# Kernel optimization log

Hardware: AMD Instinct MI355X
Metric: run time of the kernel (lower is better)

## Reference

```python
import jax, jax.numpy as jnp
import numpy as np

E = 512
H = 8
D = E // H
HID = 2048
NE = 4
TOPK = 2
EPS = 1e-5
NEG = -1e9


def _ln(x, w, b):
    mu = jnp.mean(x, axis=-1, keepdims=True)
    var = jnp.mean(jnp.square(x - mu), axis=-1, keepdims=True)
    return (x - mu) * jax.lax.rsqrt(var + EPS) * w + b


def _expert(xf, mask, ln1_w, ln1_b, ipw, ipb, opw, opb, ln2_w, ln2_b, w1, b1, w2, b2):
    # xf: [T, E]; mask: [T] bool (allowed keys = routed tokens)
    T = xf.shape[0]
    h = _ln(xf, ln1_w, ln1_b)
    qkv = h @ ipw.T + ipb                       # [T, 3E]
    q, k, v = jnp.split(qkv, 3, axis=-1)
    q = q.reshape(T, H, D).transpose(1, 0, 2)   # [H, T, D]
    k = k.reshape(T, H, D).transpose(1, 0, 2)
    v = v.reshape(T, H, D).transpose(1, 0, 2)
    scores = jnp.einsum('htd,hsd->hts', q, k) / jnp.sqrt(jnp.asarray(D, xf.dtype))
    scores = jnp.where(mask[None, None, :], scores, NEG)
    a = jax.nn.softmax(scores, axis=-1)
    o = jnp.einsum('hts,hsd->htd', a, v).transpose(1, 0, 2).reshape(T, E)
    o = o @ opw.T + opb
    x1 = xf + o                                 # residual (dropout = identity, eval)
    h2 = _ln(x1, ln2_w, ln2_b)
    m = jax.nn.gelu(h2 @ w1.T + b1, approximate=False) @ w2.T + b2
    return x1 + m


def setup_inputs() -> dict:
    key = jax.random.key(0)
    ks = jax.random.split(key, 16)
    s = 0.02
    inp = {
        'x': jax.random.normal(ks[0], (4, 512, E), dtype=jnp.float32),
        'gate_w': jax.random.normal(ks[1], (NE, E), dtype=jnp.float32) * s,
        'gate_b': jnp.zeros((NE,), jnp.float32),
        'ln1_w': jnp.ones((NE, E), jnp.float32),
        'ln1_b': jnp.zeros((NE, E), jnp.float32),
        'in_proj_w': jax.random.normal(ks[2], (NE, 3 * E, E), dtype=jnp.float32) * s,
        'in_proj_b': jnp.zeros((NE, 3 * E), jnp.float32),
        'out_proj_w': jax.random.normal(ks[3], (NE, E, E), dtype=jnp.float32) * s,
        'out_proj_b': jnp.zeros((NE, E), jnp.float32),
        'ln2_w': jnp.ones((NE, E), jnp.float32),
        'ln2_b': jnp.zeros((NE, E), jnp.float32),
        'mlp_w1': jax.random.normal(ks[4], (NE, HID, E), dtype=jnp.float32) * s,
        'mlp_b1': jnp.zeros((NE, HID), jnp.float32),
        'mlp_w2': jax.random.normal(ks[5], (NE, E, HID), dtype=jnp.float32) * s,
        'mlp_b2': jnp.zeros((NE, E), jnp.float32),
    }
    return inp


def reference(x, gate_w, gate_b, ln1_w, ln1_b, in_proj_w, in_proj_b, out_proj_w,
              out_proj_b, ln2_w, ln2_b, mlp_w1, mlp_b1, mlp_w2, mlp_b2):
    B, N, _ = x.shape
    T = B * N
    xf = x.reshape(T, E)
    logits = xf @ gate_w.T + gate_b                      # [T, NE]
    topk_val, topk_idx = jax.lax.top_k(logits, TOPK)
    probs = jax.nn.softmax(topk_val, axis=-1)            # [T, TOPK]
    out = jnp.zeros_like(xf)
    for kk in range(TOPK):
        idx = topk_idx[:, kk]
        w = probs[:, kk][:, None]
        for e in range(NE):
            mask = idx == e
            eo = _expert(xf, mask,
                         ln1_w[e], ln1_b[e], in_proj_w[e], in_proj_b[e],
                         out_proj_w[e], out_proj_b[e], ln2_w[e], ln2_b[e],
                         mlp_w1[e], mlp_b1[e], mlp_w2[e], mlp_b2[e])
            out = out + jnp.where(mask[:, None], eo * w, 0.0)
    return out.reshape(B, N, E)
```

## Files before the change

kernel.cpp:

```cpp
#include <hip/hip_runtime.h>
#include <hip/hip_bf16.h>

#define T_TOK 2048
#define E_DIM 512
#define NHEAD 8
#define DHEAD 64
#define HID_D 2048
#define NEXP 4
#define NROW_ (2 * T_TOK)
#define VT_STRIDE 4352

typedef short short8 __attribute__((ext_vector_type(8)));
typedef float floatx4 __attribute__((ext_vector_type(4)));

__device__ __forceinline__ void gld16(const void* g, void* l) {
  __builtin_amdgcn_global_load_lds((const __attribute__((address_space(1))) void*)g,
                                   (__attribute__((address_space(3))) void*)l, 16, 0, 0);
}

__device__ inline float wave_sum(float v) {
  for (int off = 32; off > 0; off >>= 1) v += __shfl_xor(v, off);
  return v;
}

__device__ __forceinline__ unsigned pack_bf2(float a, float b) {
  __hip_bfloat16 ha = __float2bfloat16(a), hb = __float2bfloat16(b);
  unsigned ua = *(unsigned short*)&ha, ub = *(unsigned short*)&hb;
  return ua | (ub << 16);
}

__device__ __forceinline__ void cvt4(const float* __restrict__ s, __hip_bfloat16* __restrict__ d,
                                     int i4, int n) {
  if (i4 < n) {
    float4 v = *reinterpret_cast<const float4*>(s + i4);
    __hip_bfloat16 tmp[4] = {__float2bfloat16(v.x), __float2bfloat16(v.y),
                             __float2bfloat16(v.z), __float2bfloat16(v.w)};
    *reinterpret_cast<ushort4*>(d + i4) = *reinterpret_cast<const ushort4*>(tmp);
  }
}

__global__ void cvt_weights(const float* __restrict__ s0, const float* __restrict__ s1,
                            const float* __restrict__ s2, const float* __restrict__ s3,
                            __hip_bfloat16* d0, __hip_bfloat16* d1,
                            __hip_bfloat16* d2, __hip_bfloat16* d3,
                            int n0, int n1, int n2, int n3) {
  int i4 = (blockIdx.x * 256 + threadIdx.x) * 4;
  cvt4(s0, d0, i4, n0);
  cvt4(s1, d1, i4, n1);
  cvt4(s2, d2, i4, n2);
  cvt4(s3, d3, i4, n3);
}

__global__ void gate_kernel(const float* __restrict__ x, const float* __restrict__ gw,
                            const float* __restrict__ gb, int* token_e, float* token_p) {
  int wid = threadIdx.x >> 6, lane = threadIdx.x & 63;
  int t = blockIdx.x * 4 + wid;
  float a0 = 0, a1 = 0, a2 = 0, a3 = 0;
  for (int i = 0; i < 8; i++) {
    int c = lane + 64 * i;
    float xv = x[(size_t)t * E_DIM + c];
    a0 += xv * gw[0 * E_DIM + c];
    a1 += xv * gw[1 * E_DIM + c];
    a2 += xv * gw[2 * E_DIM + c];
    a3 += xv * gw[3 * E_DIM + c];
  }
  a0 = wave_sum(a0); a1 = wave_sum(a1); a2 = wave_sum(a2); a3 = wave_sum(a3);
  if (lane == 0) {
    float lg[4] = {a0 + gb[0], a1 + gb[1], a2 + gb[2], a3 + gb[3]};
    int i0 = 0;
    for (int e = 1; e < 4; e++) if (lg[e] > lg[i0]) i0 = e;
    int i1 = -1;
    for (int e = 0; e < 4; e++) {
      if (e == i0) continue;
      if (i1 < 0 || lg[e] > lg[i1]) i1 = e;
    }
    float e1 = __expf(lg[i1] - lg[i0]);
    float inv = 1.f / (1.f + e1);
    token_e[t] = i0; token_e[T_TOK + t] = i1;
    token_p[t] = inv; token_p[T_TOK + t] = e1 * inv;
  }
}

__global__ void count_kernel(const int* __restrict__ token_e, int* counts) {
  int g = blockIdx.x, kk = g >> 2, e = g & 3;
  __shared__ int ws4[4];
  int tid = threadIdx.x, wid = tid >> 6, lane = tid & 63;
  int c = 0;
  for (int t = tid; t < T_TOK; t += 256) c += (token_e[kk * T_TOK + t] == e);
  for (int off = 32; off; off >>= 1) c += __shfl_xor(c, off);
  if (lane == 0) ws4[wid] = c;
  __syncthreads();
  if (tid == 0) counts[g] = ws4[0] + ws4[1] + ws4[2] + ws4[3];
}

__global__ void offs_kernel(const int* __restrict__ counts, int* offs, int* padoffs) {
  int o = 0, po = 0;
  offs[0] = 0; padoffs[0] = 0;
  for (int g = 0; g < 8; g++) {
    o += counts[g]; offs[g + 1] = o;
    po += (counts[g] + 31) & ~31; padoffs[g + 1] = po;
  }
}

__global__ void compact_kernel(const int* __restrict__ token_e, const int* __restrict__ offs,
                               const int* __restrict__ padoffs, int* perm, int* rowg,
                               int* pmap, int* invrow) {
  int g = blockIdx.x, kk = g >> 2, e = g & 3;
  __shared__ int wcnt[4];
  __shared__ int base;
  int tid = threadIdx.x, wid = tid >> 6, lane = tid & 63;
  int og = offs[g], pg = padoffs[g];
  if (tid == 0) base = 0;
  __syncthreads();
  for (int t0 = 0; t0 < T_TOK; t0 += 256) {
    int t = t0 + tid;
    bool pred = token_e[kk * T_TOK + t] == e;
    unsigned long long mask = __ballot(pred);
    int rank = __popcll(mask & ((1ull << lane) - 1ull));
    if (lane == 0) wcnt[wid] = __popcll(mask);
    __syncthreads();
    int woff = 0;
    for (int i = 0; i < wid; i++) woff += wcnt[i];
    if (pred) {
      int row = og + base + woff + rank;
      perm[row] = t;
      rowg[row] = g;
      pmap[row] = pg + (row - og);
      invrow[kk * T_TOK + t] = row;
    }
    __syncthreads();
    if (tid == 0) base += wcnt[0] + wcnt[1] + wcnt[2] + wcnt[3];
    __syncthreads();
  }
}

__global__ void ln_kernel(const float* __restrict__ src, const int* __restrict__ perm,
                          const int* __restrict__ rowg, const float* __restrict__ lnw,
                          const float* __restrict__ lnb, __hip_bfloat16* __restrict__ dst) {
  int wid = threadIdx.x >> 6, lane = threadIdx.x & 63;
  int row = blockIdx.x * 4 + wid;
  int e = rowg[row] & 3;
  const float* xr = src + (size_t)(perm ? perm[row] : row) * E_DIM;
  float v[8];
  float s = 0;
  for (int i = 0; i < 8; i++) { v[i] = xr[lane + 64 * i]; s += v[i]; }
  s = wave_sum(s);
  float mu = s * (1.f / 512.f);
  float q = 0;
  for (int i = 0; i < 8; i++) { float d = v[i] - mu; q += d * d; }
  q = wave_sum(q);
  float rstd = rsqrtf(q * (1.f / 512.f) + 1e-5f);
  for (int i = 0; i < 8; i++) {
    int c = lane + 64 * i;
    dst[(size_t)row * E_DIM + c] =
        __float2bfloat16((v[i] - mu) * rstd * lnw[e * E_DIM + c] + lnb[e * E_DIM + c]);
  }
}

__global__ void transpose_v(const short* __restrict__ v, const int* __restrict__ pmap,
                            short* __restrict__ vT) {
  __shared__ short tile[64][65];
  int r0 = blockIdx.x * 64, c0 = blockIdx.y * 64;
  int tc = threadIdx.x & 63, tr4 = threadIdx.x >> 6;
  for (int i = 0; i < 64; i += 4)
    tile[tr4 + i][tc] = v[(size_t)(r0 + tr4 + i) * E_DIM + c0 + tc];
  __syncthreads();
  int pcol = pmap[r0 + tc];
  for (int i = 0; i < 64; i += 4)
    vT[(size_t)(c0 + tr4 + i) * VT_STRIDE + pcol] = tile[tc][tr4 + i];
}

__global__ void zero_gaps(const int* __restrict__ offs, const int* __restrict__ padoffs,
                          short* __restrict__ vT) {
  int g = blockIdx.x;
  int cnt = offs[g + 1] - offs[g];
  int gap = (padoffs[g + 1] - padoffs[g]) - cnt;
  if ((int)threadIdx.x < gap) {
    int col = padoffs[g] + cnt + threadIdx.x;
    for (int d = blockIdx.y; d < E_DIM; d += gridDim.y)
      vT[(size_t)d * VT_STRIDE + col] = 0;
  }
}

__global__ __launch_bounds__(256) void attn_mfma(
    const short* __restrict__ qb, const short* __restrict__ kb,
    const short* __restrict__ vT, const int* __restrict__ offs,
    const int* __restrict__ padoffs, __hip_bfloat16* __restrict__ ob) {
  int d0 = blockIdx.x;
  int g = d0 & 7;
  int rem = d0 >> 3;
  int h = rem >> 5;
  int qblk = rem & 31;
  int sbeg = offs[g], rend = offs[g + 1];
  int q0 = sbeg + qblk * 64;
  if (q0 >= rend) return;
  int G = rend - sbeg;
  int pg = padoffs[g];
  int tid = threadIdx.x, wid = tid >> 6, lane = tid & 63;
  int fr = lane & 15, lg = lane >> 4;
  int qw = q0 + wid * 16;

  __shared__ short Kt[2][32 * 64];
  __shared__ short Vt[2][64 * 32];

  int arow = qw + fr; if (arow > rend - 1) arow = rend - 1;
  const short* qp = qb + (size_t)arow * E_DIM + h * DHEAD;
  short8 qf0 = *reinterpret_cast<const short8*>(qp + lg * 8);
  short8 qf1 = *reinterpret_cast<const short8*>(qp + 32 + lg * 8);

  int offB = tid * 16;
  int krow = offB >> 7, kinner = offB & 127;
  int ksrc = (kinner ^ ((krow & 7) << 4)) >> 1;
  int vL = offB ^ (((offB >> 7) & 7) << 4);
  int vd = vL >> 6, vkey0 = (vL & 63) >> 1;
  int wb = wid * 512;
  const short* vrow = vT + (size_t)(h * DHEAD + vd) * VT_STRIDE + pg;

  auto stage = [&](int buf, int kbase) {
    int gr = sbeg + kbase + krow; if (gr > NROW_ - 1) gr = NROW_ - 1;
    gld16(kb + (size_t)gr * E_DIM + h * DHEAD + ksrc, &Kt[buf][wb]);
    gld16(vrow + kbase + vkey0, &Vt[buf][wb]);
  };

  floatx4 acc[4] = {};
  float m_r = -1e30f, l_r = 0.f;

  stage(0, 0);
  asm volatile("s_waitcnt vmcnt(0)" ::: "memory");
  __syncthreads();

  int cur = 0;
  for (int kbase = 0; kbase < G; kbase += 32) {
    if (kbase + 32 < G) stage(cur ^ 1, kbase + 32);
    const char* Kb = (const char*)&Kt[cur][0];
    const char* Vb = (const char*)&Vt[cur][0];

    int r0r = fr, r1r = 16 + fr;
    short8 kf00 = *reinterpret_cast<const short8*>(Kb + r0r * 128 + ((lg * 16) ^ ((r0r & 7) << 4)));
    short8 kf01 = *reinterpret_cast<const short8*>(Kb + r0r * 128 + ((64 + lg * 16) ^ ((r0r & 7) << 4)));
    short8 kf10 = *reinterpret_cast<const short8*>(Kb + r1r * 128 + ((lg * 16) ^ ((r1r & 7) << 4)));
    short8 kf11 = *reinterpret_cast<const short8*>(Kb + r1r * 128 + ((64 + lg * 16) ^ ((r1r & 7) << 4)));

    floatx4 s0 = {}, s1 = {};
    s0 = __builtin_amdgcn_mfma_f32_16x16x32_bf16(kf00, qf0, s0, 0, 0, 0);
    s0 = __builtin_amdgcn_mfma_f32_16x16x32_bf16(kf01, qf1, s0, 0, 0, 0);
    s1 = __builtin_amdgcn_mfma_f32_16x16x32_bf16(kf10, qf0, s1, 0, 0, 0);
    s1 = __builtin_amdgcn_mfma_f32_16x16x32_bf16(kf11, qf1, s1, 0, 0, 0);

    float sv[8];
    float mloc = -1e30f;
#pragma unroll
    for (int j = 0; j < 4; j++) {
      int k0 = kbase + lg * 4 + j;
      sv[j] = (k0 < G) ? s0[j] * 0.125f : -1e30f;
      sv[4 + j] = (k0 + 16 < G) ? s1[j] * 0.125f : -1e30f;
      mloc = fmaxf(mloc, fmaxf(sv[j], sv[4 + j]));
    }
    mloc = fmaxf(mloc, __shfl_xor(mloc, 16));
    mloc = fmaxf(mloc, __shfl_xor(mloc, 32));
    if (__any(mloc > m_r + 8.f)) {
      float mn = fmaxf(m_r, mloc);
      float corr = __expf(m_r - mn);
      m_r = mn;
      l_r *= corr;
      float cq0 = __shfl(corr, lg * 4 + 0), cq1 = __shfl(corr, lg * 4 + 1);
      float cq2 = __shfl(corr, lg * 4 + 2), cq3 = __shfl(corr, lg * 4 + 3);
#pragma unroll
      for (int db = 0; db < 4; db++) {
        acc[db][0] *= cq0; acc[db][1] *= cq1; acc[db][2] *= cq2; acc[db][3] *= cq3;
      }
    }
    float p[8], sl = 0.f;
#pragma unroll
    for (int i = 0; i < 8; i++) { p[i] = __expf(sv[i] - m_r); sl += p[i]; }
    sl += __shfl_xor(sl, 16);
    sl += __shfl_xor(sl, 32);
    l_r += sl;

    union { unsigned u[4]; short8 s8; } pa0, pa1;
    pa0.u[0] = pack_bf2(p[0], p[1]); pa0.u[1] = pack_bf2(p[2], p[3]);
    pa0.u[2] = 0; pa0.u[3] = 0;
    pa1.u[0] = pack_bf2(p[4], p[5]); pa1.u[1] = pack_bf2(p[6], p[7]);
    pa1.u[2] = 0; pa1.u[3] = 0;

#pragma unroll
    for (int db = 0; db < 4; db++) {
      int dd = db * 16 + fr;
      int s = ((dd >> 1) & 7) << 4;
      uint2 w0 = *reinterpret_cast<const uint2*>(Vb + ((dd * 64 + lg * 8) ^ s));
      uint2 w1 = *reinterpret_cast<const uint2*>(Vb + ((dd * 64 + 32 + lg * 8) ^ s));
      union { unsigned u[4]; short8 s8; } bv0, bv1;
      bv0.u[0] = w0.x; bv0.u[1] = w0.y; bv0.u[2] = 0; bv0.u[3] = 0;
      bv1.u[0] = w1.x; bv1.u[1] = w1.y; bv1.u[2] = 0; bv1.u[3] = 0;
      acc[db] = __builtin_amdgcn_mfma_f32_16x16x32_bf16(pa0.s8, bv0.s8, acc[db], 0, 0, 0);
      acc[db] = __builtin_amdgcn_mfma_f32_16x16x32_bf16(pa1.s8, bv1.s8, acc[db], 0, 0, 0);
    }

    asm volatile("s_waitcnt vmcnt(0)" ::: "memory");
    __syncthreads();
    cur ^= 1;
  }

  float lq0 = __shfl(l_r, lg * 4 + 0), lq1 = __shfl(l_r, lg * 4 + 1);
  float lq2 = __shfl(l_r, lg * 4 + 2), lq3 = __shfl(l_r, lg * 4 + 3);
  float lq[4] = {lq0, lq1, lq2, lq3};
#pragma unroll
  for (int db = 0; db < 4; db++)
#pragma unroll
    for (int j = 0; j < 4; j++) {
      int row = qw + lg * 4 + j;
      if (row < rend)
        ob[(size_t)row * E_DIM + h * DHEAD + db * 16 + fr] = __float2bfloat16(acc[db][j] / lq[j]);
    }
}

template <int MODE>
__global__ __launch_bounds__(256) void gemm_mfma(
    const short* __restrict__ A, const short* __restrict__ Wb,
    const float* __restrict__ bias, const int* __restrict__ offs,
    const int* __restrict__ perm, const float* __restrict__ resid,
    __hip_bfloat16* __restrict__ bq, __hip_bfloat16* __restrict__ bk,
    __hip_bfloat16* __restrict__ bv, float* __restrict__ outf,
    float* __restrict__ outf2) {
  constexpr int K = (MODE == 3) ? HID_D : E_DIM;
  constexpr int N = (MODE == 0) ? 3 * E_DIM : (MODE == 2) ? HID_D : E_DIM;
  constexpr bool SPLIT = (MODE == 3);
  constexpr int KLEN = SPLIT ? K / 2 : K;
  constexpr int NKSTEP = KLEN / 64;
  constexpr int NXB = 32;
  __shared__ short Abuf[3][4096];
  __shared__ short Bbuf[3][4096];

  int d = blockIdx.x;
  int g = d & 7;
  int rem = d >> 3;
  int ksel = 0;
  if constexpr (SPLIT) { ksel = rem & 1; rem >>= 1; }
  int yb = rem / NXB, xb = rem % NXB;
  int e = g & 3;
  int rbeg = offs[g], rend = offs[g + 1];
  int row0 = rbeg + xb * 64;
  if (row0 >= rend) return;
  int col0 = yb * 64;
  int kbeg = ksel * KLEN;
  int tid = threadIdx.x;
  int wid = tid >> 6, lane = tid & 63;
  int wm = wid >> 1, wn = wid & 1;
  int fr = lane & 15, lg = lane >> 4;
  const short* wbase = Wb + (size_t)e * N * K;

  int st_row[2], st_src[2], st_arow[2];
  int wavebase = wid << 9;
  for (int c = 0; c < 2; c++) {
    int off = c * 4096 + tid * 16;
    int trow = off >> 7;
    int inner = off & 127;
    st_row[c] = trow;
    st_src[c] = (inner ^ ((trow & 7) << 4)) >> 1;
    int ga = row0 + trow;
    st_arow[c] = ga < rend ? ga : rend - 1;
  }

  auto stage = [&](int buf, int kb) {
#pragma unroll
    for (int c = 0; c < 2; c++) {
      gld16(A + (size_t)st_arow[c] * K + kb + st_src[c], &Abuf[buf][c * 2048 + wavebase]);
      gld16(wbase + (size_t)(col0 + st_row[c]) * K + kb + st_src[c],
            &Bbuf[buf][c * 2048 + wavebase]);
    }
  };

  floatx4 acc[2][2] = {};
  stage(0, kbeg);
  stage(1, kbeg + 64);
  asm volatile("s_waitcnt vmcnt(4)" ::: "memory");
  __builtin_amdgcn_s_barrier();
  __builtin_amdgcn_sched_barrier(0);

  int bcur = 0;
  for (int t = 0; t < NKSTEP; ++t) {
    int b2 = bcur + 2; if (b2 >= 3) b2 -= 3;
    if (t + 2 < NKSTEP) stage(b2, kbeg + (t + 2) * 64);
    const char* Ab = (const char*)&Abuf[bcur][0];
    const char* Bb = (const char*)&Bbuf[bcur][0];
    short8 af[2][2], bf8[2][2];
#pragma unroll
    for (int mi = 0; mi < 2; mi++)
#pragma unroll
      for (int ks = 0; ks < 2; ks++) {
        int row = wm * 32 + mi * 16 + fr;
        int cb = ks * 64 + lg * 16;
        af[mi][ks] = *reinterpret_cast<const short8*>(Ab + row * 128 + (cb ^ ((row & 7) << 4)));
      }
#pragma unroll
    for (int ni = 0; ni < 2; ni++)
#pragma unroll
      for (int ks = 0; ks < 2; ks++) {
        int row = wn * 32 + ni * 16 + fr;
        int cb = ks * 64 + lg * 16;
        bf8[ni][ks] = *reinterpret_cast<const short8*>(Bb + row * 128 + (cb ^ ((row & 7) << 4)));
      }
#pragma unroll
    for (int mi = 0; mi < 2; mi++)
#pragma unroll
      for (int ni = 0; ni < 2; ni++) {
        acc[mi][ni] = __builtin_amdgcn_mfma_f32_16x16x32_bf16(af[mi][0], bf8[ni][0], acc[mi][ni], 0, 0, 0);
        acc[mi][ni] = __builtin_amdgcn_mfma_f32_16x16x32_bf16(af[mi][1], bf8[ni][1], acc[mi][ni], 0, 0, 0);
      }
    if (t + 1 < NKSTEP) {
      if (t + 2 < NKSTEP) asm volatile("s_waitcnt vmcnt(4)" ::: "memory");
      else                asm volatile("s_waitcnt vmcnt(0)" ::: "memory");
      asm volatile("s_waitcnt lgkmcnt(0)" ::: "memory");
      __builtin_amdgcn_s_barrier();
      __builtin_amdgcn_sched_barrier(0);
    }
    bcur = (bcur + 1 == 3) ? 0 : bcur + 1;
  }

  for (int mi = 0; mi < 2; mi++)
    for (int ni = 0; ni < 2; ni++)
      for (int j = 0; j < 4; j++) {
        int row = row0 + wm * 32 + mi * 16 + lg * 4 + j;
        if (row >= rend) continue;
        int col = col0 + wn * 32 + ni * 16 + fr;
        float val = acc[mi][ni][j];
        if constexpr (MODE != 3) val += bias[e * N + col];
        if constexpr (MODE == 0) {
          if (col < E_DIM) bq[(size_t)row * E_DIM + col] = __float2bfloat16(val);
          else if (col < 2 * E_DIM) bk[(size_t)row * E_DIM + col - E_DIM] = __float2bfloat16(val);
          else bv[(size_t)row * E_DIM + col - 2 * E_DIM] = __float2bfloat16(val);
        } else if constexpr (MODE == 1) {
          int t = perm[row];
          outf[(size_t)row * E_DIM + col] = val + resid[(size_t)t * E_DIM + col];
        } else if constexpr (MODE == 2) {
          float gl = 0.5f * val * (1.f + erff(val * 0.70710678118654752f));
          bq[(size_t)row * HID_D + col] = __float2bfloat16(gl);
        } else {
          if (ksel == 0) {
            val += bias[e * N + col] + resid[(size_t)row * E_DIM + col];
            outf[(size_t)row * E_DIM + col] = val;
          } else {
            outf2[(size_t)row * E_DIM + col] = val;
          }
        }
      }
}

__global__ void combine_kernel(const float* __restrict__ y1, const float* __restrict__ y2,
                               const int* __restrict__ invrow,
                               const float* __restrict__ token_p, float* __restrict__ out) {
  int t = blockIdx.x;
  int r0 = invrow[t], r1 = invrow[T_TOK + t];
  float p0 = token_p[t], p1 = token_p[T_TOK + t];
  const float* a0 = y1 + (size_t)r0 * E_DIM;
  const float* b0 = y2 + (size_t)r0 * E_DIM;
  const float* a1 = y1 + (size_t)r1 * E_DIM;
  const float* b1 = y2 + (size_t)r1 * E_DIM;
  float* o = out + (size_t)t * E_DIM;
  for (int i = threadIdx.x; i < E_DIM; i += 256)
    o[i] = p0 * (a0[i] + b0[i]) + p1 * (a1[i] + b1[i]);
}

extern "C" void kernel_launch(void* const* d_in, const int* in_sizes, int n_in,
                              void* d_out, int out_size, void* d_ws, size_t ws_size,
                              hipStream_t stream) {
  const float* x      = (const float*)d_in[0];
  const float* gate_w = (const float*)d_in[1];
  const float* gate_b = (const float*)d_in[2];
  const float* ln1_w  = (const float*)d_in[3];
  const float* ln1_b  = (const float*)d_in[4];
  const float* ipw    = (const float*)d_in[5];
  const float* ipb    = (const float*)d_in[6];
  const float* opw    = (const float*)d_in[7];
  const float* opb    = (const float*)d_in[8];
  const float* ln2_w  = (const float*)d_in[9];
  const float* ln2_b  = (const float*)d_in[10];
  const float* w1     = (const float*)d_in[11];
  const float* b1     = (const float*)d_in[12];
  const float* w2     = (const float*)d_in[13];
  const float* b2     = (const float*)d_in[14];
  float* out = (float*)d_out;

  const int SZ_IP = NEXP * 3 * E_DIM * E_DIM;
  const int SZ_OP = NEXP * E_DIM * E_DIM;
  const int SZ_W1 = NEXP * HID_D * E_DIM;
  const int SZ_W2 = NEXP * E_DIM * HID_D;
  const int NROW = NROW_;

  char* ws = (char*)d_ws;
  size_t off = 0;
  auto carve = [&](size_t bytes) -> void* {
    void* p = ws + off;
    off += (bytes + 255) & ~(size_t)255;
    return p;
  };
  __hip_bfloat16* ipw_bf = (__hip_bfloat16*)carve((size_t)SZ_IP * 2);
  __hip_bfloat16* opw_bf = (__hip_bfloat16*)carve((size_t)SZ_OP * 2);
  __hip_bfloat16* w1_bf  = (__hip_bfloat16*)carve((size_t)SZ_W1 * 2);
  __hip_bfloat16* w2_bf  = (__hip_bfloat16*)carve((size_t)SZ_W2 * 2);
  __hip_bfloat16* h_bf   = (__hip_bfloat16*)carve((size_t)NROW * E_DIM * 2);
  __hip_bfloat16* q_bf   = (__hip_bfloat16*)carve((size_t)NROW * E_DIM * 2);
  __hip_bfloat16* k_bf   = (__hip_bfloat16*)carve((size_t)NROW * E_DIM * 2);
  __hip_bfloat16* v_bf   = (__hip_bfloat16*)carve((size_t)NROW * E_DIM * 2);
  __hip_bfloat16* o_bf   = (__hip_bfloat16*)carve((size_t)NROW * E_DIM * 2);
  __hip_bfloat16* h2_bf  = (__hip_bfloat16*)carve((size_t)NROW * E_DIM * 2);
  __hip_bfloat16* mid_bf = (__hip_bfloat16*)carve((size_t)NROW * HID_D * 2);
  short* vT     = (short*)carve((size_t)E_DIM * VT_STRIDE * 2);
  float* x1     = (float*)carve((size_t)NROW * E_DIM * 4);
  int* token_e  = (int*)carve((size_t)NROW * 4);
  float* token_p= (float*)carve((size_t)NROW * 4);
  int* perm     = (int*)carve((size_t)NROW * 4);
  int* rowg     = (int*)carve((size_t)NROW * 4);
  int* pmap     = (int*)carve((size_t)NROW * 4);
  int* invrow   = (int*)carve((size_t)NROW * 4);
  int* counts   = (int*)carve(8 * 4);
  int* offs     = (int*)carve(9 * 4);
  int* padoffs  = (int*)carve(9 * 4);
  float* ybuf  = (float*)h_bf;
  float* ybuf2 = (float*)k_bf;

  cvt_weights<<<SZ_W1 / 4 / 256, 256, 0, stream>>>(ipw, opw, w1, w2, ipw_bf, opw_bf,
                                                   w1_bf, w2_bf, SZ_IP, SZ_OP, SZ_W1, SZ_W2);
  gate_kernel<<<T_TOK / 4, 256, 0, stream>>>(x, gate_w, gate_b, token_e, token_p);
  count_kernel<<<8, 256, 0, stream>>>(token_e, counts);
  offs_kernel<<<1, 1, 0, stream>>>(counts, offs, padoffs);
  compact_kernel<<<8, 256, 0, stream>>>(token_e, offs, padoffs, perm, rowg, pmap, invrow);
  ln_kernel<<<NROW / 4, 256, 0, stream>>>(x, perm, rowg, ln1_w, ln1_b, h_bf);
  gemm_mfma<0><<<8 * 24 * 32, 256, 0, stream>>>((const short*)h_bf, (const short*)ipw_bf,
      ipb, offs, perm, nullptr, q_bf, k_bf, v_bf, nullptr, nullptr);
  transpose_v<<<dim3(NROW / 64, E_DIM / 64), 256, 0, stream>>>((const short*)v_bf, pmap, vT);
  zero_gaps<<<dim3(8, 64), 32, 0, stream>>>(offs, padoffs, vT);
  attn_mfma<<<8 * 8 * 32, 256, 0, stream>>>((const short*)q_bf, (const short*)k_bf,
      vT, offs, padoffs, o_bf);
  gemm_mfma<1><<<8 * 8 * 32, 256, 0, stream>>>((const short*)o_bf, (const short*)opw_bf,
      opb, offs, perm, x, nullptr, nullptr, nullptr, x1, nullptr);
  ln_kernel<<<NROW / 4, 256, 0, stream>>>(x1, nullptr, rowg, ln2_w, ln2_b, h2_bf);
  gemm_mfma<2><<<8 * 32 * 32, 256, 0, stream>>>((const short*)h2_bf, (const short*)w1_bf,
      b1, offs, perm, nullptr, mid_bf, nullptr, nullptr, nullptr, nullptr);
  gemm_mfma<3><<<8 * 2 * 8 * 32, 256, 0, stream>>>((const short*)mid_bf, (const short*)w2_bf,
      b2, offs, perm, x1, nullptr, nullptr, nullptr, ybuf, ybuf2);
  combine_kernel<<<T_TOK, 256, 0, stream>>>(ybuf, ybuf2, invrow, token_p, out);
  (void)in_sizes; (void)n_in; (void)ws_size;
}
```

Baseline: 183.6 us.

## Triple-buffer 64-key attention tiles, fuse routing kernels, vectorise combine

The attention kernel now processes 64 keys per iteration with a three-stage LDS ring, prefetching two tiles ahead with partial vmcnt waits and raising wave priority around the MFMA sections. This cuts barrier and loop overhead per key and hides more load latency. The count, offset and compact kernels are merged into one route kernel that each block recomputes redundantly, removing two launches. The combine kernel switches to float4 with 128 threads, and the vT padding moves to 64-row alignment, which needs zero_gaps widened to 64 threads. The larger LDS footprint may lower occupancy.

```diff
diff --git a/kernel.cpp b/kernel.cpp
--- a/kernel.cpp
+++ b/kernel.cpp
@@ -8,7 +8,7 @@
 #define HID_D 2048
 #define NEXP 4
 #define NROW_ (2 * T_TOK)
-#define VT_STRIDE 4352
+#define VT_STRIDE 4608
 
 typedef short short8 __attribute__((ext_vector_type(8)));
 typedef float floatx4 __attribute__((ext_vector_type(4)));
@@ -81,35 +81,30 @@
   }
 }
 
-__global__ void count_kernel(const int* __restrict__ token_e, int* counts) {
+__global__ void route_kernel(const int* __restrict__ token_e, int* perm, int* rowg,
+                             int* pmap, int* invrow, int* offs_out, int* padoffs_out) {
   int g = blockIdx.x, kk = g >> 2, e = g & 3;
-  __shared__ int ws4[4];
   int tid = threadIdx.x, wid = tid >> 6, lane = tid & 63;
-  int c = 0;
-  for (int t = tid; t < T_TOK; t += 256) c += (token_e[kk * T_TOK + t] == e);
-  for (int off = 32; off; off >>= 1) c += __shfl_xor(c, off);
-  if (lane == 0) ws4[wid] = c;
+  __shared__ int cnt_s[8][4];
+  for (int gg = 0; gg < 8; gg++) {
+    int kk2 = gg >> 2, e2 = gg & 3;
+    int c = 0;
+    for (int t = tid; t < T_TOK; t += 256) c += (token_e[kk2 * T_TOK + t] == e2);
+    for (int off = 32; off; off >>= 1) c += __shfl_xor(c, off);
+    if (lane == 0) cnt_s[gg][wid] = c;
+  }
   __syncthreads();
-  if (tid == 0) counts[g] = ws4[0] + ws4[1] + ws4[2] + ws4[3];
-}
-
-__global__ void offs_kernel(const int* __restrict__ counts, int* offs, int* padoffs) {
-  int o = 0, po = 0;
+  int offs[9], padoffs[9];
   offs[0] = 0; padoffs[0] = 0;
-  for (int g = 0; g < 8; g++) {
-    o += counts[g]; offs[g + 1] = o;
-    po += (counts[g] + 31) & ~31; padoffs[g + 1] = po;
-  }
-}
-
-__global__ void compact_kernel(const int* __restrict__ token_e, const int* __restrict__ offs,
-                               const int* __restrict__ padoffs, int* perm, int* rowg,
-                               int* pmap, int* invrow) {
-  int g = blockIdx.x, kk = g >> 2, e = g & 3;
+  for (int gg = 0; gg < 8; gg++) {
+    int c = cnt_s[gg][0] + cnt_s[gg][1] + cnt_s[gg][2] + cnt_s[gg][3];
+    offs[gg + 1] = offs[gg] + c;
+    padoffs[gg + 1] = padoffs[gg] + ((c + 63) & ~63);
+  }
+  if (g == 0 && tid < 9) { offs_out[tid] = offs[tid]; padoffs_out[tid] = padoffs[tid]; }
+  int og = offs[g], pg = padoffs[g];
   __shared__ int wcnt[4];
   __shared__ int base;
-  int tid = threadIdx.x, wid = tid >> 6, lane = tid & 63;
-  int og = offs[g], pg = padoffs[g];
   if (tid == 0) base = 0;
   __syncthreads();
   for (int t0 = 0; t0 < T_TOK; t0 += 256) {
@@ -200,62 +195,78 @@
   int fr = lane & 15, lg = lane >> 4;
   int qw = q0 + wid * 16;
 
-  __shared__ short Kt[2][32 * 64];
-  __shared__ short Vt[2][64 * 32];
+  __shared__ short Kt[3][64 * 64];
+  __shared__ short Vt[3][64 * 64];
 
   int arow = qw + fr; if (arow > rend - 1) arow = rend - 1;
   const short* qp = qb + (size_t)arow * E_DIM + h * DHEAD;
   short8 qf0 = *reinterpret_cast<const short8*>(qp + lg * 8);
   short8 qf1 = *reinterpret_cast<const short8*>(qp + 32 + lg * 8);
 
-  int offB = tid * 16;
-  int krow = offB >> 7, kinner = offB & 127;
-  int ksrc = (kinner ^ ((krow & 7) << 4)) >> 1;
-  int vL = offB ^ (((offB >> 7) & 7) << 4);
-  int vd = vL >> 6, vkey0 = (vL & 63) >> 1;
-  int wb = wid * 512;
-  const short* vrow = vT + (size_t)(h * DHEAD + vd) * VT_STRIDE + pg;
+  int st_row[2], st_src[2];
+  int wb = wid << 9;
+  for (int c = 0; c < 2; c++) {
+    int off = c * 4096 + tid * 16;
+    int row = off >> 7, inner = off & 127;
+    st_row[c] = row;
+    st_src[c] = (inner ^ ((row & 7) << 4)) >> 1;
+  }
 
   auto stage = [&](int buf, int kbase) {
-    int gr = sbeg + kbase + krow; if (gr > NROW_ - 1) gr = NROW_ - 1;
-    gld16(kb + (size_t)gr * E_DIM + h * DHEAD + ksrc, &Kt[buf][wb]);
-    gld16(vrow + kbase + vkey0, &Vt[buf][wb]);
+#pragma unroll
+    for (int c = 0; c < 2; c++) {
+      int gr = sbeg + kbase + st_row[c]; if (gr > NROW_ - 1) gr = NROW_ - 1;
+      gld16(kb + (size_t)gr * E_DIM + h * DHEAD + st_src[c], &Kt[buf][c * 2048 + wb]);
+      gld16(vT + (size_t)(h * DHEAD + st_row[c]) * VT_STRIDE + pg + kbase + st_src[c],
+            &Vt[buf][c * 2048 + wb]);
+    }
   };
 
   floatx4 acc[4] = {};
   float m_r = -1e30f, l_r = 0.f;
+  int nt = (G + 63) >> 6;
 
   stage(0, 0);
-  asm volatile("s_waitcnt vmcnt(0)" ::: "memory");
-  __syncthreads();
-
-  int cur = 0;
-  for (int kbase = 0; kbase < G; kbase += 32) {
-    if (kbase + 32 < G) stage(cur ^ 1, kbase + 32);
-    const char* Kb = (const char*)&Kt[cur][0];
-    const char* Vb = (const char*)&Vt[cur][0];
-
-    int r0r = fr, r1r = 16 + fr;
-    short8 kf00 = *reinterpret_cast<const short8*>(Kb + r0r * 128 + ((lg * 16) ^ ((r0r & 7) << 4)));
-    short8 kf01 = *reinterpret_cast<const short8*>(Kb + r0r * 128 + ((64 + lg * 16) ^ ((r0r & 7) << 4)));
-    short8 kf10 = *reinterpret_cast<const short8*>(Kb + r1r * 128 + ((lg * 16) ^ ((r1r & 7) << 4)));
-    short8 kf11 = *reinterpret_cast<const short8*>(Kb + r1r * 128 + ((64 + lg * 16) ^ ((r1r & 7) << 4)));
-
-    floatx4 s0 = {}, s1 = {};
-    s0 = __builtin_amdgcn_mfma_f32_16x16x32_bf16(kf00, qf0, s0, 0, 0, 0);
-    s0 = __builtin_amdgcn_mfma_f32_16x16x32_bf16(kf01, qf1, s0, 0, 0, 0);
-    s1 = __builtin_amdgcn_mfma_f32_16x16x32_bf16(kf10, qf0, s1, 0, 0, 0);
-    s1 = __builtin_amdgcn_mfma_f32_16x16x32_bf16(kf11, qf1, s1, 0, 0, 0);
-
-    float sv[8];
+  if (nt > 1) stage(1, 64);
+  if (nt > 1) asm volatile("s_waitcnt vmcnt(4)" ::: "memory");
+  else        asm volatile("s_waitcnt vmcnt(0)" ::: "memory");
+  __builtin_amdgcn_s_barrier();
+  __builtin_amdgcn_sched_barrier(0);
+
+  int bcur = 0;
+  for (int t = 0; t < nt; ++t) {
+    int kbase = t * 64;
+    int b2 = bcur + 2; if (b2 >= 3) b2 -= 3;
+    if (t + 2 < nt) stage(b2, kbase + 128);
+    const char* Kb = (const char*)&Kt[bcur][0];
+    const char* Vb = (const char*)&Vt[bcur][0];
+
+    floatx4 s[4];
+    __builtin_amdgcn_s_setprio(1);
+#pragma unroll
+    for (int c = 0; c < 4; c++) {
+      int rc = c * 16 + fr;
+      int sx = (rc & 7) << 4;
+      short8 kf0 = *reinterpret_cast<const short8*>(Kb + rc * 128 + ((lg * 16) ^ sx));
+      short8 kf1 = *reinterpret_cast<const short8*>(Kb + rc * 128 + ((64 + lg * 16) ^ sx));
+      floatx4 z = {};
+      z = __builtin_amdgcn_mfma_f32_16x16x32_bf16(kf0, qf0, z, 0, 0, 0);
+      z = __builtin_amdgcn_mfma_f32_16x16x32_bf16(kf1, qf1, z, 0, 0, 0);
+      s[c] = z;
+    }
+    __builtin_amdgcn_s_setprio(0);
+
+    float sv[16];
     float mloc = -1e30f;
 #pragma unroll
-    for (int j = 0; j < 4; j++) {
-      int k0 = kbase + lg * 4 + j;
-      sv[j] = (k0 < G) ? s0[j] * 0.125f : -1e30f;
-      sv[4 + j] = (k0 + 16 < G) ? s1[j] * 0.125f : -1e30f;
-      mloc = fmaxf(mloc, fmaxf(sv[j], sv[4 + j]));
-    }
+    for (int c = 0; c < 4; c++)
+#pragma unroll
+      for (int j = 0; j < 4; j++) {
+        int k0 = kbase + c * 16 + lg * 4 + j;
+        float v = (k0 < G) ? s[c][j] * 0.125f : -1e30f;
+        sv[c * 4 + j] = v;
+        mloc = fmaxf(mloc, v);
+      }
     mloc = fmaxf(mloc, __shfl_xor(mloc, 16));
     mloc = fmaxf(mloc, __shfl_xor(mloc, 32));
     if (__any(mloc > m_r + 8.f)) {
@@ -270,35 +281,43 @@
         acc[db][0] *= cq0; acc[db][1] *= cq1; acc[db][2] *= cq2; acc[db][3] *= cq3;
       }
     }
-    float p[8], sl = 0.f;
-#pragma unroll
-    for (int i = 0; i < 8; i++) { p[i] = __expf(sv[i] - m_r); sl += p[i]; }
+    float p[16], sl = 0.f;
+#pragma unroll
+    for (int i = 0; i < 16; i++) { p[i] = __expf(sv[i] - m_r); sl += p[i]; }
     sl += __shfl_xor(sl, 16);
     sl += __shfl_xor(sl, 32);
     l_r += sl;
 
-    union { unsigned u[4]; short8 s8; } pa0, pa1;
-    pa0.u[0] = pack_bf2(p[0], p[1]); pa0.u[1] = pack_bf2(p[2], p[3]);
-    pa0.u[2] = 0; pa0.u[3] = 0;
-    pa1.u[0] = pack_bf2(p[4], p[5]); pa1.u[1] = pack_bf2(p[6], p[7]);
-    pa1.u[2] = 0; pa1.u[3] = 0;
-
+    union { unsigned u[4]; short8 s8; } pa[4];
+#pragma unroll
+    for (int c = 0; c < 4; c++) {
+      pa[c].u[0] = pack_bf2(p[c * 4 + 0], p[c * 4 + 1]);
+      pa[c].u[1] = pack_bf2(p[c * 4 + 2], p[c * 4 + 3]);
+      pa[c].u[2] = 0; pa[c].u[3] = 0;
+    }
+    __builtin_amdgcn_s_setprio(1);
 #pragma unroll
     for (int db = 0; db < 4; db++) {
       int dd = db * 16 + fr;
-      int s = ((dd >> 1) & 7) << 4;
-      uint2 w0 = *reinterpret_cast<const uint2*>(Vb + ((dd * 64 + lg * 8) ^ s));
-      uint2 w1 = *reinterpret_cast<const uint2*>(Vb + ((dd * 64 + 32 + lg * 8) ^ s));
-      union { unsigned u[4]; short8 s8; } bv0, bv1;
-      bv0.u[0] = w0.x; bv0.u[1] = w0.y; bv0.u[2] = 0; bv0.u[3] = 0;
-      bv1.u[0] = w1.x; bv1.u[1] = w1.y; bv1.u[2] = 0; bv1.u[3] = 0;
-      acc[db] = __builtin_amdgcn_mfma_f32_16x16x32_bf16(pa0.s8, bv0.s8, acc[db], 0, 0, 0);
-      acc[db] = __builtin_amdgcn_mfma_f32_16x16x32_bf16(pa1.s8, bv1.s8, acc[db], 0, 0, 0);
-    }
-
-    asm volatile("s_waitcnt vmcnt(0)" ::: "memory");
-    __syncthreads();
-    cur ^= 1;
+      int sx = (dd & 7) << 4;
+#pragma unroll
+      for (int c = 0; c < 4; c++) {
+        uint2 w = *reinterpret_cast<const uint2*>(Vb + ((dd * 128 + c * 32 + lg * 8) ^ sx));
+        union { unsigned u[4]; short8 s8; } bv;
+        bv.u[0] = w.x; bv.u[1] = w.y; bv.u[2] = 0; bv.u[3] = 0;
+        acc[db] = __builtin_amdgcn_mfma_f32_16x16x32_bf16(pa[c].s8, bv.s8, acc[db], 0, 0, 0);
+      }
+    }
+    __builtin_amdgcn_s_setprio(0);
+
+    if (t + 1 < nt) {
+      if (t + 2 < nt) asm volatile("s_waitcnt vmcnt(4)" ::: "memory");
+      else            asm volatile("s_waitcnt vmcnt(0)" ::: "memory");
+      asm volatile("s_waitcnt lgkmcnt(0)" ::: "memory");
+      __builtin_amdgcn_s_barrier();
+      __builtin_amdgcn_sched_barrier(0);
+    }
+    bcur = bcur + 1; if (bcur == 3) bcur = 0;
   }
 
   float lq0 = __shfl(l_r, lg * 4 + 0), lq1 = __shfl(l_r, lg * 4 + 1);
@@ -452,13 +471,19 @@
   int t = blockIdx.x;
   int r0 = invrow[t], r1 = invrow[T_TOK + t];
   float p0 = token_p[t], p1 = token_p[T_TOK + t];
-  const float* a0 = y1 + (size_t)r0 * E_DIM;
-  const float* b0 = y2 + (size_t)r0 * E_DIM;
-  const float* a1 = y1 + (size_t)r1 * E_DIM;
-  const float* b1 = y2 + (size_t)r1 * E_DIM;
-  float* o = out + (size_t)t * E_DIM;
-  for (int i = threadIdx.x; i < E_DIM; i += 256)
-    o[i] = p0 * (a0[i] + b0[i]) + p1 * (a1[i] + b1[i]);
+  const float4* a0 = (const float4*)(y1 + (size_t)r0 * E_DIM);
+  const float4* b0 = (const float4*)(y2 + (size_t)r0 * E_DIM);
+  const float4* a1 = (const float4*)(y1 + (size_t)r1 * E_DIM);
+  const float4* b1 = (const float4*)(y2 + (size_t)r1 * E_DIM);
+  float4* o = (float4*)(out + (size_t)t * E_DIM);
+  int i = threadIdx.x;
+  float4 va0 = a0[i], vb0 = b0[i], va1 = a1[i], vb1 = b1[i];
+  float4 r;
+  r.x = p0 * (va0.x + vb0.x) + p1 * (va1.x + vb1.x);
+  r.y = p0 * (va0.y + vb0.y) + p1 * (va1.y + vb1.y);
+  r.z = p0 * (va0.z + vb0.z) + p1 * (va1.z + vb1.z);
+  r.w = p0 * (va0.w + vb0.w) + p1 * (va1.w + vb1.w);
+  o[i] = r;
 }
 
 extern "C" void kernel_launch(void* const* d_in, const int* in_sizes, int n_in,
@@ -513,7 +538,6 @@
   int* rowg     = (int*)carve((size_t)NROW * 4);
   int* pmap     = (int*)carve((size_t)NROW * 4);
   int* invrow   = (int*)carve((size_t)NROW * 4);
-  int* counts   = (int*)carve(8 * 4);
   int* offs     = (int*)carve(9 * 4);
   int* padoffs  = (int*)carve(9 * 4);
   float* ybuf  = (float*)h_bf;
@@ -522,14 +546,12 @@
   cvt_weights<<<SZ_W1 / 4 / 256, 256, 0, stream>>>(ipw, opw, w1, w2, ipw_bf, opw_bf,
                                                    w1_bf, w2_bf, SZ_IP, SZ_OP, SZ_W1, SZ_W2);
   gate_kernel<<<T_TOK / 4, 256, 0, stream>>>(x, gate_w, gate_b, token_e, token_p);
-  count_kernel<<<8, 256, 0, stream>>>(token_e, counts);
-  offs_kernel<<<1, 1, 0, stream>>>(counts, offs, padoffs);
-  compact_kernel<<<8, 256, 0, stream>>>(token_e, offs, padoffs, perm, rowg, pmap, invrow);
+  route_kernel<<<8, 256, 0, stream>>>(token_e, perm, rowg, pmap, invrow, offs, padoffs);
   ln_kernel<<<NROW / 4, 256, 0, stream>>>(x, perm, rowg, ln1_w, ln1_b, h_bf);
   gemm_mfma<0><<<8 * 24 * 32, 256, 0, stream>>>((const short*)h_bf, (const short*)ipw_bf,
       ipb, offs, perm, nullptr, q_bf, k_bf, v_bf, nullptr, nullptr);
   transpose_v<<<dim3(NROW / 64, E_DIM / 64), 256, 0, stream>>>((const short*)v_bf, pmap, vT);
-  zero_gaps<<<dim3(8, 64), 32, 0, stream>>>(offs, padoffs, vT);
+  zero_gaps<<<dim3(8, 64), 64, 0, stream>>>(offs, padoffs, vT);
   attn_mfma<<<8 * 8 * 32, 256, 0, stream>>>((const short*)q_bf, (const short*)k_bf,
       vT, offs, padoffs, o_bf);
   gemm_mfma<1><<<8 * 8 * 32, 256, 0, stream>>>((const short*)o_bf, (const short*)opw_bf,
@@ -539,6 +561,6 @@
       b1, offs, perm, nullptr, mid_bf, nullptr, nullptr, nullptr, nullptr);
   gemm_mfma<3><<<8 * 2 * 8 * 32, 256, 0, stream>>>((const short*)mid_bf, (const short*)w2_bf,
       b2, offs, perm, x1, nullptr, nullptr, nullptr, ybuf, ybuf2);
-  combine_kernel<<<T_TOK, 256, 0, stream>>>(ybuf, ybuf2, invrow, token_p, out);
+  combine_kernel<<<T_TOK, 128, 0, stream>>>(ybuf, ybuf2, invrow, token_p, out);
   (void)in_sizes; (void)n_in; (void)ws_size;
 }
```

Result: faster. 176.3 us (-4.0%).
